# Kernel optimization log

Measured on AMD Instinct MI355X. Metric: run time of the kernel, lower is better.

## Reference

```python
import jax, jax.numpy as jnp
import numpy as np

C = 32          # d_model / channels
D_STATE = 32
D_CONV = 4
EXPAND = 2
D_INNER = EXPAND * C          # 64
DT_RANK = (C + 15) // 16      # ceil(32/16) = 2
EPS = 1e-5


def _conv2d(x, w, b):
    # x: (B,C,H,W), w: (O,I,3,3), stride 1, padding 1 (torch Conv2d)
    y = jax.lax.conv_general_dilated(
        x, w, window_strides=(1, 1), padding=[(1, 1), (1, 1)],
        dimension_numbers=("NCHW", "OIHW", "NCHW"))
    return y + b[None, :, None, None]


def _silu(x):
    return x * jax.nn.sigmoid(x)


def _mamba(xs, in_proj_w, conv1d_w, conv1d_b, x_proj_w, dt_proj_w, dt_proj_b,
           A_log, Dp, out_proj_w):
    # xs: (B, L, C)
    xz = xs @ in_proj_w.T                       # (B, L, 2*D_INNER)
    xm, z = jnp.split(xz, 2, axis=-1)           # each (B, L, D_INNER)

    # causal depthwise conv1d along L (torch: padding=d_conv-1 then [..., :L])
    xc = xm.transpose(0, 2, 1)                  # (B, D_INNER, L)
    xc = jax.lax.conv_general_dilated(
        xc, conv1d_w, window_strides=(1,), padding=[(D_CONV - 1, 0)],
        dimension_numbers=("NCH", "OIH", "NCH"),
        feature_group_count=D_INNER)
    xm = _silu((xc + conv1d_b[None, :, None]).transpose(0, 2, 1))  # (B,L,D_INNER)

    x_dbl = xm @ x_proj_w.T                     # (B, L, DT_RANK + 2*D_STATE)
    dt = x_dbl[..., :DT_RANK]
    Bm = x_dbl[..., DT_RANK:DT_RANK + D_STATE]  # (B, L, N)
    Cm = x_dbl[..., DT_RANK + D_STATE:]         # (B, L, N)

    delta = jax.nn.softplus(dt @ dt_proj_w.T + dt_proj_b)  # (B, L, D_INNER)
    A = -jnp.exp(A_log)                                     # (D_INNER, N)

    deltaA = jnp.exp(delta[..., None] * A)                           # (B,L,D,N)
    deltaBx = delta[..., None] * Bm[:, :, None, :] * xm[..., None]   # (B,L,D,N)

    def combine(c1, c2):
        a1, b1 = c1
        a2, b2 = c2
        return a1 * a2, a2 * b1 + b2

    # parallel linear recurrence h_t = deltaA_t * h_{t-1} + deltaBx_t
    _, hstate = jax.lax.associative_scan(combine, (deltaA, deltaBx), axis=1)

    y = jnp.einsum("bldn,bln->bld", hstate, Cm) + xm * Dp
    y = y * _silu(z)
    return y @ out_proj_w.T                     # (B, L, C)


def setup_inputs() -> dict:
    key = jax.random.key(0)
    ks = jax.random.split(key, 16)
    s = 0.02
    inp = {
        "x": jax.random.normal(ks[0], (4, C, 64, 64), dtype=jnp.float32),
        "conv1_w": jax.random.normal(ks[1], (2 * C, C, 3, 3), jnp.float32) * s,
        "conv1_b": jnp.zeros((2 * C,), jnp.float32),
        "conv2_w": jax.random.normal(ks[2], (C, 2 * C, 3, 3), jnp.float32) * s,
        "conv2_b": jnp.zeros((C,), jnp.float32),
        "ln_g": jnp.ones((C,), jnp.float32),
        "ln_b": jnp.zeros((C,), jnp.float32),
        "in_proj_w": jax.random.normal(ks[3], (2 * D_INNER, C), jnp.float32) * s,
        "conv1d_w": jax.random.normal(ks[4], (D_INNER, 1, D_CONV), jnp.float32) * 0.1,
        "conv1d_b": jnp.zeros((D_INNER,), jnp.float32),
        "x_proj_w": jax.random.normal(ks[5], (DT_RANK + 2 * D_STATE, D_INNER), jnp.float32) * s,
        "dt_proj_w": jax.random.normal(ks[6], (D_INNER, DT_RANK), jnp.float32) * 0.1,
        "dt_proj_b": jax.random.normal(ks[7], (D_INNER,), jnp.float32) * 0.1 - 4.0,
        "A_log": jnp.log(jnp.tile(jnp.arange(1, D_STATE + 1, dtype=jnp.float32), (D_INNER, 1))),
        "Dp": jnp.ones((D_INNER,), jnp.float32),
        "out_proj_w": jax.random.normal(ks[8], (C, D_INNER), jnp.float32) * s,
        "smooth_w": jax.random.normal(ks[9], (C, C, 3, 3), jnp.float32) * s,
        "smooth_b": jnp.zeros((C,), jnp.float32),
    }
    return inp


def reference(x, conv1_w, conv1_b, conv2_w, conv2_b, ln_g, ln_b,
              in_proj_w, conv1d_w, conv1d_b, x_proj_w, dt_proj_w, dt_proj_b,
              A_log, Dp, out_proj_w, smooth_w, smooth_b):
    b, c, h, w = x.shape
    # convb residual
    t = jax.nn.relu(_conv2d(x, conv1_w, conv1_b))
    x = _conv2d(t, conv2_w, conv2_b) + x
    # reshape (b,c,h,w) -> (b, h*w, c) row-major (faithful to torch .reshape)
    xs = x.reshape(b, -1, c)
    # LayerNorm over last dim
    mu = jnp.mean(xs, axis=-1, keepdims=True)
    var = jnp.mean(jnp.square(xs - mu), axis=-1, keepdims=True)
    xs = (xs - mu) * jax.lax.rsqrt(var + EPS) * ln_g + ln_b
    # Mamba block
    y = _mamba(xs, in_proj_w, conv1d_w, conv1d_b, x_proj_w, dt_proj_w,
               dt_proj_b, A_log, Dp, out_proj_w)
    y = y.transpose(0, 2, 1).reshape(b, c, h, w)
    return _conv2d(y, smooth_w, smooth_b)
```

## Files before the change

### kernel.cpp

```cpp
#include <hip/hip_runtime.h>
#include <math.h>

#define SEQL 4096
#define L2E 1.44269504088896340736f

#if defined(__has_builtin)
#if __has_builtin(__builtin_amdgcn_exp2f)
#define FAST_EXP2(x) __builtin_amdgcn_exp2f(x)
#endif
#endif
#ifndef FAST_EXP2
#define FAST_EXP2(x) exp2f(x)
#endif

__device__ __forceinline__ float sigmoid_f(float x){ return 1.0f/(1.0f+expf(-x)); }

template<int CI, int CO, int COG, bool RELU, bool RES>
__global__ __launch_bounds__(256) void conv3x3_k(const float* __restrict__ in,
    const float* __restrict__ wgt, const float* __restrict__ bias,
    const float* __restrict__ res, float* __restrict__ out)
{
  constexpr int CIT = CI/4;
  __shared__ float tin[4][2][6][72];
  __shared__ float red[3][4][COG][66];
  const int tid  = threadIdx.x;
  const int lane = tid & 63;
  const int ty   = tid >> 6;
  const int h0   = blockIdx.x * 4;
  const int co0  = blockIdx.y * COG;
  const int b    = blockIdx.z;

  if (lane < 24){
    int cl = lane / 12, rem = lane % 12, r = rem >> 1, side = rem & 1;
    tin[ty][cl][r][side ? 68 : 3] = 0.0f;
  }

  float acc[4][COG];
  #pragma unroll
  for (int rr=0;rr<4;++rr)
    #pragma unroll
    for (int u=0;u<COG;++u) acc[rr][u] = 0.0f;

  const int ci0 = ty*CIT;
  for (int cig = ci0; cig < ci0 + CIT; cig += 2){
    #pragma unroll
    for (int k=0;k<3;++k){
      int idx4 = lane + (k<<6);
      int row  = idx4 >> 4;
      int cl = row/6, r = row - cl*6;
      int w4 = (idx4 & 15) << 2;
      int h  = h0 - 1 + r;
      float4 v = make_float4(0.f,0.f,0.f,0.f);
      if (h>=0 && h<64)
        v = *(const float4*)(in + ((size_t)(b*CI+cig+cl)*64 + h)*64 + w4);
      *(float4*)&tin[ty][cl][r][4+w4] = v;
    }
    #pragma unroll
    for (int cl=0; cl<2; ++cl){
      float rv[6][3];
      #pragma unroll
      for (int r=0;r<6;++r)
        #pragma unroll
        for (int c=0;c<3;++c)
          rv[r][c] = tin[ty][cl][r][3+lane+c];
      #pragma unroll
      for (int u=0;u<COG;++u){
        const float* wp = wgt + ((size_t)(co0+u)*CI + cig + cl)*9;
        #pragma unroll
        for (int rr=0;rr<4;++rr)
          #pragma unroll
          for (int j=0;j<3;++j){
            acc[rr][u] = fmaf(rv[rr+j][0], wp[3*j+0], acc[rr][u]);
            acc[rr][u] = fmaf(rv[rr+j][1], wp[3*j+1], acc[rr][u]);
            acc[rr][u] = fmaf(rv[rr+j][2], wp[3*j+2], acc[rr][u]);
          }
      }
    }
  }
  if (ty > 0){
    #pragma unroll
    for (int rr=0;rr<4;++rr)
      #pragma unroll
      for (int u=0;u<COG;++u) red[ty-1][rr][u][lane] = acc[rr][u];
  }
  __syncthreads();
  if (ty == 0){
    #pragma unroll
    for (int rr=0;rr<4;++rr)
      #pragma unroll
      for (int u=0;u<COG;++u){
        float s = acc[rr][u] + red[0][rr][u][lane] + red[1][rr][u][lane]
                + red[2][rr][u][lane] + bias[co0+u];
        size_t ob = ((size_t)(b*CO+co0+u)*64 + h0+rr)*64 + lane;
        if constexpr (RES)  s += res[ob];
        if constexpr (RELU) s = fmaxf(s, 0.0f);
        out[ob] = s;
      }
  }
}

__global__ __launch_bounds__(1024) void mamba_in_k(const float* __restrict__ x2,
    const float* __restrict__ g, const float* __restrict__ be,
    const float* __restrict__ Wip, const float* __restrict__ cw,
    const float* __restrict__ cb, const float* __restrict__ Wxp,
    const float* __restrict__ Wdt, const float* __restrict__ bdt,
    const float* __restrict__ A_log,
    float* __restrict__ xm2, float* __restrict__ szb, float* __restrict__ dlt,
    float* __restrict__ Bm, float* __restrict__ Cm,
    float* __restrict__ cA, float* __restrict__ cH)
{
  __shared__ float xn[68][37];
  __shared__ float xm[64][68];
  __shared__ float xt[64][67];
  __shared__ float xd[64][67];
  const int tid = threadIdx.x, lane = tid & 63, ty = tid >> 6;
  const int bi = blockIdx.x >> 6;
  const int l0 = (blockIdx.x & 63) << 6;

  if (ty < 2){
    int t = ty*64 + lane;
    if (t < 67){
      int tok = l0 - 3 + t;
      if (tok >= 0){
        const float* row = x2 + (size_t)bi*131072 + (size_t)tok*32;
        float v[32];
        #pragma unroll
        for (int c=0;c<32;c+=4){
          float4 f = *(const float4*)(row + c);
          v[c]=f.x; v[c+1]=f.y; v[c+2]=f.z; v[c+3]=f.w;
        }
        float p[8];
        #pragma unroll
        for (int j2=0;j2<8;++j2) p[j2]=v[j2];
        #pragma unroll
        for (int i=8;i<32;i+=8){
          #pragma unroll
          for (int j2=0;j2<8;++j2) p[j2]+=v[i+j2];
        }
        float mu = (((p[0]+p[1])+(p[2]+p[3]))+((p[4]+p[5])+(p[6]+p[7]))) * 0.03125f;
        float q[8];
        #pragma unroll
        for (int j2=0;j2<8;++j2){ float dd=v[j2]-mu; q[j2]=dd*dd; }
        #pragma unroll
        for (int i=8;i<32;i+=8){
          #pragma unroll
          for (int j2=0;j2<8;++j2){ float dd=v[i+j2]-mu; q[j2]+=dd*dd; }
        }
        float var = (((q[0]+q[1])+(q[2]+q[3]))+((q[4]+q[5])+(q[6]+q[7]))) * 0.03125f;
        float rstd = 1.0f / sqrtf(var + 1e-5f);
        #pragma unroll
        for (int c=0;c<32;++c) xn[t][c] = (v[c]-mu)*rstd*g[c] + be[c];
      } else {
        #pragma unroll
        for (int c=0;c<32;++c) xn[t][c] = 0.0f;
      }
    }
  }
  __syncthreads();

  if (ty < 8){
    const int d0 = ty*8;
    float xvA[32];
    #pragma unroll
    for (int c=0;c<32;++c) xvA[c] = xn[lane][c];
    #pragma unroll
    for (int jj=0;jj<8;++jj){
      const float* wr = Wip + (d0+jj)*32;
      float a = 0.0f;
      #pragma unroll
      for (int c=0;c<32;++c) a = fmaf(xvA[c], wr[c], a);
      xm[d0+jj][lane] = a;
    }
    if (lane < 3){
      float xvB[32];
      #pragma unroll
      for (int c=0;c<32;++c) xvB[c] = xn[64+lane][c];
      #pragma unroll
      for (int jj=0;jj<8;++jj){
        const float* wr = Wip + (d0+jj)*32;
        float a = 0.0f;
        #pragma unroll
        for (int c=0;c<32;++c) a = fmaf(xvB[c], wr[c], a);
        xm[d0+jj][64+lane] = a;
      }
    }
  } else {
    const int d0z = (ty-8)*8;
    float xvC[32];
    #pragma unroll
    for (int c=0;c<32;++c) xvC[c] = xn[lane+3][c];
    #pragma unroll
    for (int jj=0;jj<8;++jj){
      const float* wr = Wip + (64+d0z+jj)*32;
      float a = 0.0f;
      #pragma unroll
      for (int c=0;c<32;++c) a = fmaf(xvC[c], wr[c], a);
      szb[((size_t)(bi*64+d0z+jj))*SEQL + l0 + lane] = a * sigmoid_f(a);
    }
  }
  __syncthreads();

  #pragma unroll
  for (int jj=0;jj<4;++jj){
    int d = ty*4 + jj;
    float a = xm[d][lane]*cw[d*4] + xm[d][lane+1]*cw[d*4+1]
            + xm[d][lane+2]*cw[d*4+2] + xm[d][lane+3]*cw[d*4+3] + cb[d];
    float s = a * sigmoid_f(a);
    xt[lane][d] = s;
    xm2[((size_t)(bi*64+d))*SEQL + l0 + lane] = s;
  }
  __syncthreads();

  {
    float xv[64];
    #pragma unroll
    for (int c=0;c<64;++c) xv[c] = xt[lane][c];
    for (int j=ty; j<66; j+=16){
      const float* wr = Wxp + j*64;
      float a = 0.0f;
      #pragma unroll
      for (int c=0;c<64;++c) a = fmaf(xv[c], wr[c], a);
      xd[lane][j] = a;
    }
  }
  __syncthreads();

  {
    float dt0 = xd[lane][0], dt1 = xd[lane][1];
    #pragma unroll
    for (int k=0;k<4;++k){
      int d2 = ty*4 + k;
      float v = dt0*Wdt[d2*2] + dt1*Wdt[d2*2+1] + bdt[d2];
      float sp = fmaxf(v,0.0f) + log1pf(expf(-fabsf(v)));
      dlt[((size_t)(bi*64+d2))*SEQL + l0 + lane] = sp;
      xm[d2][lane] = sp;
    }
    const int which = ty >> 3, gq = ty & 7;
    float* dst = which ? Cm : Bm;
    size_t base = ((size_t)bi*SEQL + l0 + lane)*32 + gq*4;
    const int s2 = 2 + which*32;
    float4 f0;
    f0.x = xd[lane][s2+gq+ 0]; f0.y = xd[lane][s2+gq+ 8];
    f0.z = xd[lane][s2+gq+16]; f0.w = xd[lane][s2+gq+24];
    *(float4*)(dst + base) = f0;
  }
  __syncthreads();

  {
    const int d  = tid >> 4;
    const int gg = tid & 15;
    const int chunk = blockIdx.x & 63;
    const int bd = bi*64 + d;
    float Av2[2], h[2] = {0,0}, aP[2] = {1,1};
    #pragma unroll
    for (int j=0;j<2;++j) Av2[j] = -expf(A_log[d*32 + gg + 16*j]) * L2E;
    #pragma unroll 4
    for (int t=0;t<64;++t){
      float dlv = xm[d][t];
      float xv2 = xt[t][d];
      #pragma unroll
      for (int j=0;j<2;++j){
        float bv = xd[t][2 + gg + 16*j];
        float a = FAST_EXP2(dlv*Av2[j]);
        h[j] = fmaf(a, h[j], dlv*bv*xv2);
        aP[j] *= a;
      }
    }
    #pragma unroll
    for (int j=0;j<2;++j){
      size_t idx = (((size_t)bd<<5) + gg + 16*j)*64 + chunk;
      cA[idx] = aP[j]; cH[idx] = h[j];
    }
  }
}

__global__ __launch_bounds__(256) void scan_p2(const float* __restrict__ dlt,
    const float* __restrict__ xssm, const float* __restrict__ Bm,
    const float* __restrict__ Cm, const float* __restrict__ A_log,
    const float* __restrict__ Dp, const float* __restrict__ sz,
    const float* __restrict__ cA, const float* __restrict__ cHs,
    float* __restrict__ yt)
{
  __shared__ float pre[32][34];
  const int tid = threadIdx.x;
  const int grp = blockIdx.x & 1;
  const int bd  = blockIdx.x >> 1;
  const int b = bd >> 6, d = bd & 63;
  const int c0 = grp << 5;

  if (tid < 32){
    const float* pa = cA  + (((size_t)bd<<5)+tid)*64;
    const float* ph = cHs + (((size_t)bd<<5)+tid)*64;
    float hrun = 0.0f;
    if (grp){
      #pragma unroll 4
      for (int c=0;c<32;c+=4){
        float4 a4 = *(const float4*)(pa+c);
        float4 h4 = *(const float4*)(ph+c);
        hrun = fmaf(a4.x,hrun,h4.x);
        hrun = fmaf(a4.y,hrun,h4.y);
        hrun = fmaf(a4.z,hrun,h4.z);
        hrun = fmaf(a4.w,hrun,h4.w);
      }
    }
    #pragma unroll 4
    for (int k=0;k<32;k+=4){
      float4 a4 = *(const float4*)(pa+c0+k);
      float4 h4 = *(const float4*)(ph+c0+k);
      pre[tid][k+0]=hrun; hrun=fmaf(a4.x,hrun,h4.x);
      pre[tid][k+1]=hrun; hrun=fmaf(a4.y,hrun,h4.y);
      pre[tid][k+2]=hrun; hrun=fmaf(a4.z,hrun,h4.z);
      pre[tid][k+3]=hrun; hrun=fmaf(a4.w,hrun,h4.w);
    }
  }
  __syncthreads();

  const int lc = tid >> 3, gg = tid & 7;
  const int chunk = c0 + lc;
  const int l0 = chunk << 6;
  const float Dv = Dp[d];
  float Av2[4], h[4];
  #pragma unroll
  for (int j=0;j<4;++j){
    Av2[j] = -expf(A_log[d*32 + gg + 8*j]) * L2E;
    h[j] = pre[gg + 8*j][lc];
  }
  const float* del = dlt  + (size_t)bd*SEQL + l0;
  const float* xp  = xssm + (size_t)bd*SEQL + l0;
  const float* szp = sz   + (size_t)bd*SEQL + l0;
  const float* Bp  = Bm + ((size_t)b*SEQL + l0)*32 + gg*4;
  const float* Cp  = Cm + ((size_t)b*SEQL + l0)*32 + gg*4;
  float* yp = yt + (size_t)bd*SEQL + l0;

  #pragma unroll 2
  for (int i0=0;i0<64;i0+=4){
    float4 d4 = *(const float4*)(del+i0);
    float4 x4 = *(const float4*)(xp +i0);
    float4 s4 = *(const float4*)(szp+i0);
    float y[4];
    #pragma unroll
    for (int t=0;t<4;++t){
      float dl = (t==0)? d4.x : (t==1)? d4.y : (t==2)? d4.z : d4.w;
      float xl = (t==0)? x4.x : (t==1)? x4.y : (t==2)? x4.z : x4.w;
      float sl = (t==0)? s4.x : (t==1)? s4.y : (t==2)? s4.z : s4.w;
      float4 bv = *(const float4*)(Bp + (i0+t)*32);
      float4 cv = *(const float4*)(Cp + (i0+t)*32);
      float a0 = FAST_EXP2(dl*Av2[0]); h[0] = fmaf(a0, h[0], dl*bv.x*xl);
      float a1 = FAST_EXP2(dl*Av2[1]); h[1] = fmaf(a1, h[1], dl*bv.y*xl);
      float a2 = FAST_EXP2(dl*Av2[2]); h[2] = fmaf(a2, h[2], dl*bv.z*xl);
      float a3 = FAST_EXP2(dl*Av2[3]); h[3] = fmaf(a3, h[3], dl*bv.w*xl);
      float v = fmaf(h[3], cv.w, fmaf(h[2], cv.z, fmaf(h[1], cv.y, h[0]*cv.x)));
      v += __shfl_xor(v,1); v += __shfl_xor(v,2); v += __shfl_xor(v,4);
      y[t] = fmaf(xl, Dv, v) * sl;
    }
    if (gg == 0)
      *(float4*)(yp + i0) = make_float4(y[0], y[1], y[2], y[3]);
  }
}

__global__ __launch_bounds__(512) void outproj_k(const float* __restrict__ yt,
    const float* __restrict__ Wout, float* __restrict__ ym)
{
  __shared__ float ys[64][67];
  const int tid = threadIdx.x, lane = tid & 63, ty = tid >> 6;
  const int bi = blockIdx.x >> 6;
  const int l0 = (blockIdx.x & 63) << 6;
  for (int r=ty; r<64; r+=8)
    ys[lane][r] = yt[((size_t)(bi*64+r))*SEQL + l0 + lane];
  __syncthreads();
  float yv[64];
  #pragma unroll
  for (int c=0;c<64;++c) yv[c] = ys[lane][c];
  #pragma unroll
  for (int jj=0;jj<4;++jj){
    int j = ty*4 + jj;
    const float* wr = Wout + j*64;
    float acc = 0.0f;
    #pragma unroll
    for (int c=0;c<64;++c) acc = fmaf(yv[c], wr[c], acc);
    ym[((size_t)(bi*32+j))*SEQL + l0 + lane] = acc;
  }
}

extern "C" void kernel_launch(void* const* d_in, const int* in_sizes, int n_in,
                              void* d_out, int out_size, void* d_ws, size_t ws_size,
                              hipStream_t stream) {
  const float* x        = (const float*)d_in[0];
  const float* conv1_w  = (const float*)d_in[1];
  const float* conv1_b  = (const float*)d_in[2];
  const float* conv2_w  = (const float*)d_in[3];
  const float* conv2_b  = (const float*)d_in[4];
  const float* ln_g     = (const float*)d_in[5];
  const float* ln_b     = (const float*)d_in[6];
  const float* in_proj_w= (const float*)d_in[7];
  const float* conv1d_w = (const float*)d_in[8];
  const float* conv1d_b = (const float*)d_in[9];
  const float* x_proj_w = (const float*)d_in[10];
  const float* dt_proj_w= (const float*)d_in[11];
  const float* dt_proj_b= (const float*)d_in[12];
  const float* A_log    = (const float*)d_in[13];
  const float* Dp       = (const float*)d_in[14];
  const float* out_proj_w=(const float*)d_in[15];
  const float* smooth_w = (const float*)d_in[16];
  const float* smooth_b = (const float*)d_in[17];
  float* out = (float*)d_out;

  float* ws = (float*)d_ws;
  float* t      = ws;
  float* x2     = t      + 1048576;
  float* xm2    = x2     + 524288;
  float* szb    = xm2    + 1048576;
  float* dlt    = szb    + 1048576;
  float* Bmat   = dlt    + 1048576;
  float* Cmat   = Bmat   + 524288;
  float* yt     = Cmat   + 524288;
  float* ym     = yt     + 1048576;
  float* cA     = t;
  float* cH     = t + 524288;

  conv3x3_k<32,64,4,true ,false><<<dim3(16,16,4), 256, 0, stream>>>(x,  conv1_w, conv1_b, nullptr, t);
  conv3x3_k<64,32,4,false,true ><<<dim3(16,8,4), 256, 0, stream>>>(t,  conv2_w, conv2_b, x,       x2);
  mamba_in_k  <<<256, 1024, 0, stream>>>(x2, ln_g, ln_b, in_proj_w, conv1d_w, conv1d_b,
                                         x_proj_w, dt_proj_w, dt_proj_b, A_log,
                                         xm2, szb, dlt, Bmat, Cmat, cA, cH);
  scan_p2     <<<512, 256, 0, stream>>>(dlt, xm2, Bmat, Cmat, A_log, Dp, szb, cA, cH, yt);
  outproj_k   <<<256, 512, 0, stream>>>(yt, out_proj_w, ym);
  conv3x3_k<32,32,4,false,false><<<dim3(16,8,4), 256, 0, stream>>>(ym, smooth_w, smooth_b, nullptr, out);
}
```

Baseline: 202.6 us.

## Halve scan chunk length to double block count across Mamba kernels

Shrinks the chunked selective-scan chunk from 64 to 32 tokens (128 chunks per sequence). The input kernel now launches 512 blocks and the second scan pass 1024 blocks, so more of the GPU's CUs have work. Phase work is remapped onto 32-token tiles, and chunk carries are stored chunk-major with cH moved to a new workspace region. The cost is a longer serial prefix over chunk carries, now done with strided scalar loads instead of float4, plus lower per-block utilisation in the 32-token phases.

```diff
diff --git a/kernel.cpp b/kernel.cpp
--- a/kernel.cpp
+++ b/kernel.cpp
@@ -2,6 +2,7 @@
 #include <math.h>
 
 #define SEQL 4096
+#define NCH 128
 #define L2E 1.44269504088896340736f
 
 #if defined(__has_builtin)
@@ -99,7 +100,7 @@
   }
 }
 
-__global__ __launch_bounds__(1024) void mamba_in_k(const float* __restrict__ x2,
+__global__ __launch_bounds__(1024, 8) void mamba_in_k(const float* __restrict__ x2,
     const float* __restrict__ g, const float* __restrict__ be,
     const float* __restrict__ Wip, const float* __restrict__ cw,
     const float* __restrict__ cb, const float* __restrict__ Wxp,
@@ -109,166 +110,164 @@
     float* __restrict__ Bm, float* __restrict__ Cm,
     float* __restrict__ cA, float* __restrict__ cH)
 {
-  __shared__ float xn[68][37];
-  __shared__ float xm[64][68];
-  __shared__ float xt[64][67];
-  __shared__ float xd[64][67];
+  __shared__ float xn[35][37];
+  __shared__ float xm[64][36];
+  __shared__ float xt[32][65];
+  __shared__ float xd[32][67];
   const int tid = threadIdx.x, lane = tid & 63, ty = tid >> 6;
-  const int bi = blockIdx.x >> 6;
-  const int l0 = (blockIdx.x & 63) << 6;
-
-  if (ty < 2){
-    int t = ty*64 + lane;
-    if (t < 67){
-      int tok = l0 - 3 + t;
-      if (tok >= 0){
-        const float* row = x2 + (size_t)bi*131072 + (size_t)tok*32;
-        float v[32];
-        #pragma unroll
-        for (int c=0;c<32;c+=4){
-          float4 f = *(const float4*)(row + c);
-          v[c]=f.x; v[c+1]=f.y; v[c+2]=f.z; v[c+3]=f.w;
-        }
-        float p[8];
-        #pragma unroll
-        for (int j2=0;j2<8;++j2) p[j2]=v[j2];
-        #pragma unroll
-        for (int i=8;i<32;i+=8){
-          #pragma unroll
-          for (int j2=0;j2<8;++j2) p[j2]+=v[i+j2];
-        }
-        float mu = (((p[0]+p[1])+(p[2]+p[3]))+((p[4]+p[5])+(p[6]+p[7]))) * 0.03125f;
-        float q[8];
-        #pragma unroll
-        for (int j2=0;j2<8;++j2){ float dd=v[j2]-mu; q[j2]=dd*dd; }
-        #pragma unroll
-        for (int i=8;i<32;i+=8){
-          #pragma unroll
-          for (int j2=0;j2<8;++j2){ float dd=v[i+j2]-mu; q[j2]+=dd*dd; }
-        }
-        float var = (((q[0]+q[1])+(q[2]+q[3]))+((q[4]+q[5])+(q[6]+q[7]))) * 0.03125f;
-        float rstd = 1.0f / sqrtf(var + 1e-5f);
-        #pragma unroll
-        for (int c=0;c<32;++c) xn[t][c] = (v[c]-mu)*rstd*g[c] + be[c];
-      } else {
-        #pragma unroll
-        for (int c=0;c<32;++c) xn[t][c] = 0.0f;
-      }
+  const int bi    = blockIdx.x >> 7;
+  const int chunk = blockIdx.x & 127;
+  const int l0    = chunk << 5;
+
+  if (tid < 35){
+    int tok = l0 - 3 + tid;
+    if (tok >= 0){
+      const float* row = x2 + (size_t)bi*131072 + (size_t)tok*32;
+      float v[32];
+      #pragma unroll
+      for (int c=0;c<32;c+=4){
+        float4 f = *(const float4*)(row + c);
+        v[c]=f.x; v[c+1]=f.y; v[c+2]=f.z; v[c+3]=f.w;
+      }
+      float p[8];
+      #pragma unroll
+      for (int j2=0;j2<8;++j2) p[j2]=v[j2];
+      #pragma unroll
+      for (int i=8;i<32;i+=8){
+        #pragma unroll
+        for (int j2=0;j2<8;++j2) p[j2]+=v[i+j2];
+      }
+      float mu = (((p[0]+p[1])+(p[2]+p[3]))+((p[4]+p[5])+(p[6]+p[7]))) * 0.03125f;
+      float q[8];
+      #pragma unroll
+      for (int j2=0;j2<8;++j2){ float dd=v[j2]-mu; q[j2]=dd*dd; }
+      #pragma unroll
+      for (int i=8;i<32;i+=8){
+        #pragma unroll
+        for (int j2=0;j2<8;++j2){ float dd=v[i+j2]-mu; q[j2]+=dd*dd; }
+      }
+      float var = (((q[0]+q[1])+(q[2]+q[3]))+((q[4]+q[5])+(q[6]+q[7]))) * 0.03125f;
+      float rstd = 1.0f / sqrtf(var + 1e-5f);
+      #pragma unroll
+      for (int c=0;c<32;++c) xn[tid][c] = (v[c]-mu)*rstd*g[c] + be[c];
+    } else {
+      #pragma unroll
+      for (int c=0;c<32;++c) xn[tid][c] = 0.0f;
     }
   }
   __syncthreads();
 
   if (ty < 8){
-    const int d0 = ty*8;
-    float xvA[32];
-    #pragma unroll
-    for (int c=0;c<32;++c) xvA[c] = xn[lane][c];
-    #pragma unroll
-    for (int jj=0;jj<8;++jj){
-      const float* wr = Wip + (d0+jj)*32;
-      float a = 0.0f;
-      #pragma unroll
-      for (int c=0;c<32;++c) a = fmaf(xvA[c], wr[c], a);
-      xm[d0+jj][lane] = a;
-    }
-    if (lane < 3){
-      float xvB[32];
-      #pragma unroll
-      for (int c=0;c<32;++c) xvB[c] = xn[64+lane][c];
+    if (lane < 35){
+      const int d0 = ty*8;
+      float xvA[32];
+      #pragma unroll
+      for (int c=0;c<32;++c) xvA[c] = xn[lane][c];
       #pragma unroll
       for (int jj=0;jj<8;++jj){
         const float* wr = Wip + (d0+jj)*32;
         float a = 0.0f;
         #pragma unroll
-        for (int c=0;c<32;++c) a = fmaf(xvB[c], wr[c], a);
-        xm[d0+jj][64+lane] = a;
+        for (int c=0;c<32;++c) a = fmaf(xvA[c], wr[c], a);
+        xm[d0+jj][lane] = a;
       }
     }
   } else {
-    const int d0z = (ty-8)*8;
-    float xvC[32];
-    #pragma unroll
-    for (int c=0;c<32;++c) xvC[c] = xn[lane+3][c];
-    #pragma unroll
-    for (int jj=0;jj<8;++jj){
-      const float* wr = Wip + (64+d0z+jj)*32;
-      float a = 0.0f;
-      #pragma unroll
-      for (int c=0;c<32;++c) a = fmaf(xvC[c], wr[c], a);
-      szb[((size_t)(bi*64+d0z+jj))*SEQL + l0 + lane] = a * sigmoid_f(a);
-    }
-  }
-  __syncthreads();
-
-  #pragma unroll
-  for (int jj=0;jj<4;++jj){
-    int d = ty*4 + jj;
-    float a = xm[d][lane]*cw[d*4] + xm[d][lane+1]*cw[d*4+1]
-            + xm[d][lane+2]*cw[d*4+2] + xm[d][lane+3]*cw[d*4+3] + cb[d];
-    float s = a * sigmoid_f(a);
-    xt[lane][d] = s;
-    xm2[((size_t)(bi*64+d))*SEQL + l0 + lane] = s;
+    if (lane < 32){
+      const int d0z = (ty-8)*8;
+      float xvC[32];
+      #pragma unroll
+      for (int c=0;c<32;++c) xvC[c] = xn[lane+3][c];
+      #pragma unroll
+      for (int jj=0;jj<8;++jj){
+        const float* wr = Wip + (64+d0z+jj)*32;
+        float a = 0.0f;
+        #pragma unroll
+        for (int c=0;c<32;++c) a = fmaf(xvC[c], wr[c], a);
+        szb[((size_t)(bi*64+d0z+jj))*SEQL + l0 + lane] = a * sigmoid_f(a);
+      }
+    }
   }
   __syncthreads();
 
   {
-    float xv[64];
-    #pragma unroll
-    for (int c=0;c<64;++c) xv[c] = xt[lane][c];
-    for (int j=ty; j<66; j+=16){
-      const float* wr = Wxp + j*64;
-      float a = 0.0f;
-      #pragma unroll
-      for (int c=0;c<64;++c) a = fmaf(xv[c], wr[c], a);
-      xd[lane][j] = a;
+    const int tok = tid & 31, dd = tid >> 5;
+    #pragma unroll
+    for (int h2=0; h2<2; ++h2){
+      int d = dd + h2*32;
+      float a = xm[d][tok]*cw[d*4] + xm[d][tok+1]*cw[d*4+1]
+              + xm[d][tok+2]*cw[d*4+2] + xm[d][tok+3]*cw[d*4+3] + cb[d];
+      float s = a * sigmoid_f(a);
+      xt[tok][d] = s;
+      xm2[((size_t)(bi*64+d))*SEQL + l0 + tok] = s;
     }
   }
   __syncthreads();
 
   {
-    float dt0 = xd[lane][0], dt1 = xd[lane][1];
-    #pragma unroll
-    for (int k=0;k<4;++k){
-      int d2 = ty*4 + k;
+    const int tok = tid & 31, jb = tid >> 5;
+    const float* w0 = Wxp + jb*64;
+    const float* w1 = Wxp + (jb+32)*64;
+    float a0 = 0.0f, a1 = 0.0f;
+    #pragma unroll
+    for (int c=0;c<64;++c){
+      float xv = xt[tok][c];
+      a0 = fmaf(xv, w0[c], a0);
+      a1 = fmaf(xv, w1[c], a1);
+    }
+    xd[tok][jb]    = a0;
+    xd[tok][jb+32] = a1;
+    if (jb < 2){
+      const float* w2 = Wxp + (64+jb)*64;
+      float a2 = 0.0f;
+      #pragma unroll
+      for (int c=0;c<64;++c) a2 = fmaf(xt[tok][c], w2[c], a2);
+      xd[tok][64+jb] = a2;
+    }
+  }
+  __syncthreads();
+
+  {
+    const int tok = tid & 31, dd = tid >> 5;
+    float dt0 = xd[tok][0], dt1 = xd[tok][1];
+    #pragma unroll
+    for (int h2=0;h2<2;++h2){
+      int d2 = dd + h2*32;
       float v = dt0*Wdt[d2*2] + dt1*Wdt[d2*2+1] + bdt[d2];
       float sp = fmaxf(v,0.0f) + log1pf(expf(-fabsf(v)));
-      dlt[((size_t)(bi*64+d2))*SEQL + l0 + lane] = sp;
-      xm[d2][lane] = sp;
-    }
-    const int which = ty >> 3, gq = ty & 7;
-    float* dst = which ? Cm : Bm;
-    size_t base = ((size_t)bi*SEQL + l0 + lane)*32 + gq*4;
-    const int s2 = 2 + which*32;
-    float4 f0;
-    f0.x = xd[lane][s2+gq+ 0]; f0.y = xd[lane][s2+gq+ 8];
-    f0.z = xd[lane][s2+gq+16]; f0.w = xd[lane][s2+gq+24];
-    *(float4*)(dst + base) = f0;
+      dlt[((size_t)(bi*64+d2))*SEQL + l0 + tok] = sp;
+      xm[d2][tok] = sp;
+    }
+    const int tok2 = tid >> 5, p = tid & 31;
+    const int src = (p>>2) + 8*(p&3);
+    size_t base = ((size_t)bi*SEQL + l0)*32;
+    Bm[base + tid] = xd[tok2][2  + src];
+    Cm[base + tid] = xd[tok2][34 + src];
   }
   __syncthreads();
 
   {
     const int d  = tid >> 4;
     const int gg = tid & 15;
-    const int chunk = blockIdx.x & 63;
     const int bd = bi*64 + d;
     float Av2[2], h[2] = {0,0}, aP[2] = {1,1};
     #pragma unroll
     for (int j=0;j<2;++j) Av2[j] = -expf(A_log[d*32 + gg + 16*j]) * L2E;
     #pragma unroll 4
-    for (int t=0;t<64;++t){
+    for (int t=0;t<32;++t){
       float dlv = xm[d][t];
-      float xv2 = xt[t][d];
+      float m   = dlv * xt[t][d];
       #pragma unroll
       for (int j=0;j<2;++j){
         float bv = xd[t][2 + gg + 16*j];
         float a = FAST_EXP2(dlv*Av2[j]);
-        h[j] = fmaf(a, h[j], dlv*bv*xv2);
+        h[j] = fmaf(a, h[j], m*bv);
         aP[j] *= a;
       }
     }
     #pragma unroll
     for (int j=0;j<2;++j){
-      size_t idx = (((size_t)bd<<5) + gg + 16*j)*64 + chunk;
+      size_t idx = ((size_t)bd*NCH + chunk)*32 + gg + 16*j;
       cA[idx] = aP[j]; cH[idx] = h[j];
     }
   }
@@ -283,41 +282,28 @@
 {
   __shared__ float pre[32][34];
   const int tid = threadIdx.x;
-  const int grp = blockIdx.x & 1;
-  const int bd  = blockIdx.x >> 1;
+  const int grp = blockIdx.x & 3;
+  const int bd  = blockIdx.x >> 2;
   const int b = bd >> 6, d = bd & 63;
   const int c0 = grp << 5;
 
   if (tid < 32){
-    const float* pa = cA  + (((size_t)bd<<5)+tid)*64;
-    const float* ph = cHs + (((size_t)bd<<5)+tid)*64;
+    const float* pa = cA  + (size_t)bd*NCH*32 + tid;
+    const float* ph = cHs + (size_t)bd*NCH*32 + tid;
     float hrun = 0.0f;
-    if (grp){
-      #pragma unroll 4
-      for (int c=0;c<32;c+=4){
-        float4 a4 = *(const float4*)(pa+c);
-        float4 h4 = *(const float4*)(ph+c);
-        hrun = fmaf(a4.x,hrun,h4.x);
-        hrun = fmaf(a4.y,hrun,h4.y);
-        hrun = fmaf(a4.z,hrun,h4.z);
-        hrun = fmaf(a4.w,hrun,h4.w);
-      }
-    }
+    for (int c=0;c<c0;++c)
+      hrun = fmaf(pa[(size_t)c*32], hrun, ph[(size_t)c*32]);
     #pragma unroll 4
-    for (int k=0;k<32;k+=4){
-      float4 a4 = *(const float4*)(pa+c0+k);
-      float4 h4 = *(const float4*)(ph+c0+k);
-      pre[tid][k+0]=hrun; hrun=fmaf(a4.x,hrun,h4.x);
-      pre[tid][k+1]=hrun; hrun=fmaf(a4.y,hrun,h4.y);
-      pre[tid][k+2]=hrun; hrun=fmaf(a4.z,hrun,h4.z);
-      pre[tid][k+3]=hrun; hrun=fmaf(a4.w,hrun,h4.w);
+    for (int k=0;k<32;++k){
+      pre[tid][k] = hrun;
+      hrun = fmaf(pa[(size_t)(c0+k)*32], hrun, ph[(size_t)(c0+k)*32]);
     }
   }
   __syncthreads();
 
   const int lc = tid >> 3, gg = tid & 7;
   const int chunk = c0 + lc;
-  const int l0 = chunk << 6;
+  const int l0 = chunk << 5;
   const float Dv = Dp[d];
   float Av2[4], h[4];
   #pragma unroll
@@ -333,7 +319,7 @@
   float* yp = yt + (size_t)bd*SEQL + l0;
 
   #pragma unroll 2
-  for (int i0=0;i0<64;i0+=4){
+  for (int i0=0;i0<32;i0+=4){
     float4 d4 = *(const float4*)(del+i0);
     float4 x4 = *(const float4*)(xp +i0);
     float4 s4 = *(const float4*)(szp+i0);
@@ -416,14 +402,14 @@
   float* yt     = Cmat   + 524288;
   float* ym     = yt     + 1048576;
   float* cA     = t;
-  float* cH     = t + 524288;
+  float* cH     = ym     + 524288;
 
   conv3x3_k<32,64,4,true ,false><<<dim3(16,16,4), 256, 0, stream>>>(x,  conv1_w, conv1_b, nullptr, t);
   conv3x3_k<64,32,4,false,true ><<<dim3(16,8,4), 256, 0, stream>>>(t,  conv2_w, conv2_b, x,       x2);
-  mamba_in_k  <<<256, 1024, 0, stream>>>(x2, ln_g, ln_b, in_proj_w, conv1d_w, conv1d_b,
+  mamba_in_k  <<<512, 1024, 0, stream>>>(x2, ln_g, ln_b, in_proj_w, conv1d_w, conv1d_b,
                                          x_proj_w, dt_proj_w, dt_proj_b, A_log,
                                          xm2, szb, dlt, Bmat, Cmat, cA, cH);
-  scan_p2     <<<512, 256, 0, stream>>>(dlt, xm2, Bmat, Cmat, A_log, Dp, szb, cA, cH, yt);
+  scan_p2     <<<1024, 256, 0, stream>>>(dlt, xm2, Bmat, Cmat, A_log, Dp, szb, cA, cH, yt);
   outproj_k   <<<256, 512, 0, stream>>>(yt, out_proj_w, ym);
   conv3x3_k<32,32,4,false,false><<<dim3(16,8,4), 256, 0, stream>>>(ym, smooth_w, smooth_b, nullptr, out);
 }
```

Result: slower. 233.0 us (+15.0%).
